# Kernel optimization log

Measured on AMD Instinct MI355X. Metric: run time of the kernel, lower is better.

Reference implementation:

```python
import jax, jax.numpy as jnp
import numpy as np

N = 4
IS_SLOW = (False, False, True, True)
RATES = (1, 1, 4, 4)
THRESH = 0.3
F2S_IDX = {(0, 2): 0, (0, 3): 1, (1, 2): 2, (1, 3): 3}


def _conv1d(x, w, stride, pad):
    # x: [B, C_in, T], w: [C_out, C_in, K]
    return jax.lax.conv_general_dilated(
        x, w, (stride,), [(pad, pad)], dimension_numbers=("NCH", "OIH", "NCH"))


def _linear_interp(x, t_out):
    # x: [B, D, T_in] -> [B, D, t_out]; matches F.interpolate(mode='linear', align_corners=False)
    t_in = x.shape[2]
    scale = t_in / t_out
    src = (jnp.arange(t_out, dtype=jnp.float32) + 0.5) * scale - 0.5
    src = jnp.clip(src, 0.0, float(t_in - 1))
    i0 = jnp.floor(src).astype(jnp.int32)
    i1 = jnp.minimum(i0 + 1, t_in - 1)
    w = (src - i0.astype(jnp.float32)).astype(x.dtype)
    return x[:, :, i0] * (1.0 - w) + x[:, :, i1] * w


def setup_inputs() -> dict:
    key = jax.random.key(0)
    ks = jax.random.split(key, 8)
    T_FAST, T_SLOW, B, D, H = 512, 128, 32, 1024, 256
    return {
        "feat0": jax.random.normal(ks[0], (T_FAST, B, D), jnp.float32),
        "feat1": jax.random.normal(ks[1], (T_FAST, B, D), jnp.float32),
        "feat2": jax.random.normal(ks[2], (T_SLOW, B, D), jnp.float32),
        "feat3": jax.random.normal(ks[3], (T_SLOW, B, D), jnp.float32),
        "mlp_w1": jax.random.normal(ks[4], (N * N, 2 * D, H), jnp.float32) * 0.02,
        "mlp_b1": jnp.zeros((N * N, H), jnp.float32),
        "mlp_w2": jax.random.normal(ks[5], (N * N, H, 1), jnp.float32) * 0.02,
        "mlp_b2": jnp.zeros((N * N, 1), jnp.float32),
        "s2f_w": jax.random.normal(ks[6], (D, D, 1), jnp.float32) * 0.02,
        "s2f_b": jnp.zeros((D,), jnp.float32),
        "f2s_w": jax.random.normal(ks[7], (4, D, D, 5), jnp.float32) * 0.02,
    }


def reference(feat0, feat1, feat2, feat3, mlp_w1, mlp_b1, mlp_w2, mlp_b2,
              s2f_w, s2f_b, f2s_w):
    feats = [feat0, feat1, feat2, feat3]            # [T_i, B, D]
    feats_bdt = [jnp.transpose(f, (1, 2, 0)) for f in feats]  # [B, D, T_i]
    globals_ = [f.mean(axis=2) for f in feats_bdt]  # [B, D]
    outputs = list(feats)
    for i in range(N):
        for j in range(N):
            if i == j:
                continue
            p = i * N + j
            pair_vec = jnp.concatenate([globals_[i], globals_[j]], axis=-1)  # [B, 2D]
            h = jax.nn.relu(pair_vec @ mlp_w1[p] + mlp_b1[p])
            score = jax.nn.sigmoid(h @ mlp_w2[p] + mlp_b2[p])[:, 0]          # [B]
            cond = score.mean() >= THRESH
            if IS_SLOW[i] and not IS_SLOW[j]:
                # slow -> fast: interpolate up, 1x1 conv proj, score-weighted residual
                up = _linear_interp(feats_bdt[i], feats_bdt[j].shape[2])
                up = _conv1d(up, s2f_w, 1, 0) + s2f_b[None, :, None]
                new = feats_bdt[j] + score[:, None, None] * up
                outputs[j] = jnp.where(cond, jnp.transpose(new, (2, 0, 1)), outputs[j])
            elif (not IS_SLOW[i]) and IS_SLOW[j]:
                # fast -> slow: strided conv down, score-weighted residual
                stride = RATES[j] // RATES[i]
                down = _conv1d(feats_bdt[i], f2s_w[F2S_IDX[(i, j)]], stride, 2)
                new = feats_bdt[j] + score[:, None, None] * down
                outputs[j] = jnp.where(cond, jnp.transpose(new, (2, 0, 1)), outputs[j])
    return tuple(outputs)
```

## Files before the change

### kernel.cpp

```cpp
#include <hip/hip_runtime.h>
#include <math.h>

typedef __bf16 bf16;
typedef bf16 bf16x8 __attribute__((ext_vector_type(8)));
typedef bf16 bf16x4 __attribute__((ext_vector_type(4)));
typedef float f32x4 __attribute__((ext_vector_type(4)));

#define OFF_GLOB   0ul
#define OFF_H      524288ul
#define OFF_SCORE  786432ul
#define OFF_COND   787456ul
#define OFF_PART   788480ul
#define OFF_PROJ   4982784ul
#define OFF_WTF2S  38537216ul
#define OFF_WTS2F  59508736ul
#define OFF_F0B    61605888ul
#define OFF_F1B    95160320ul
#define OFF_F2B    128714752ul
#define OFF_F3B    137103360ul
#define WS_NEED    145491968ul


__device__ __forceinline__ void slot_ij(int s, int& i, int& j) {
  if (s < 4) { i = 2 + (s & 1); j = s >> 1; }
  else       { int ss = s - 4; i = ss & 1; j = 2 + (ss >> 1); }
}

__global__ __launch_bounds__(256) void k_means_part(
    const float* __restrict__ f0, const float* __restrict__ f1,
    const float* __restrict__ f2, const float* __restrict__ f3,
    float* __restrict__ part,
    bf16* __restrict__ b0, bf16* __restrict__ b1,
    bf16* __restrict__ b2, bf16* __restrict__ b3, int do_conv)
{
  int b = blockIdx.x, c = blockIdx.y, i = blockIdx.z, tid = threadIdx.x;
  const float* f = (i == 0) ? f0 : (i == 1) ? f1 : (i == 2) ? f2 : f3;
  bf16* fb = (i == 0) ? b0 : (i == 1) ? b1 : (i == 2) ? b2 : b3;
  int chunk = (i < 2) ? 64 : 16;
  int t0 = c * chunk;
  float4 s = make_float4(0.f, 0.f, 0.f, 0.f);
  for (int t = t0; t < t0 + chunk; ++t) {
    float4 v = ((const float4*)(f + (size_t)(t * 32 + b) * 1024))[tid];
    s.x += v.x; s.y += v.y; s.z += v.z; s.w += v.w;
    if (do_conv) {
      bf16x4 o;
      o[0] = (bf16)v.x; o[1] = (bf16)v.y; o[2] = (bf16)v.z; o[3] = (bf16)v.w;
      *(bf16x4*)(fb + (size_t)(t * 32 + b) * 1024 + tid * 4) = o;
    }
  }
  ((float4*)part)[(size_t)((i * 8 + c) * 32 + b) * 256 + tid] = s;
}

__global__ __launch_bounds__(256) void k_means_final(
    const float* __restrict__ part, float* __restrict__ g)
{
  int b = blockIdx.x, i = blockIdx.y, tid = threadIdx.x;
  float4 s = make_float4(0.f, 0.f, 0.f, 0.f);
  for (int c = 0; c < 8; ++c) {
    float4 v = ((const float4*)part)[(size_t)((i * 8 + c) * 32 + b) * 256 + tid];
    s.x += v.x; s.y += v.y; s.z += v.z; s.w += v.w;
  }
  float inv = (i < 2) ? (1.f / 512.f) : (1.f / 128.f);
  s.x *= inv; s.y *= inv; s.z *= inv; s.w *= inv;
  ((float4*)g)[(size_t)(i * 32 + b) * 256 + tid] = s;
}

__global__ __launch_bounds__(256) void k_mlp1(
    const float* __restrict__ g, const float* __restrict__ w1, float* __restrict__ h_ws)
{
  int s = blockIdx.x, hc = blockIdx.y, kz = blockIdx.z, tid = threadIdx.x;
  int pi, pj; slot_ij(s, pi, pj);
  int p = pi * 4 + pj;
  int h = hc * 32 + (tid & 31);
  int bg = tid >> 5;
  __shared__ float pv[32 * 65];
  float acc0 = 0.f, acc1 = 0.f, acc2 = 0.f, acc3 = 0.f;
  for (int kt = 0; kt < 8; ++kt) {
    int k0 = kz * 512 + kt * 64;
    __syncthreads();
    for (int l = tid; l < 2048; l += 256) {
      int bb = l >> 6, kk = l & 63;
      int k = k0 + kk;
      float v = (k < 1024) ? g[(size_t)pi * 32768 + bb * 1024 + k]
                           : g[(size_t)pj * 32768 + bb * 1024 + (k - 1024)];
      pv[bb * 65 + kk] = v;
    }
    __syncthreads();
    const float* wp = w1 + ((size_t)p * 2048 + k0) * 256 + hc * 32 + (tid & 31);
    for (int kk = 0; kk < 64; ++kk) {
      float w = wp[(size_t)kk * 256];
      acc0 += pv[(bg * 4 + 0) * 65 + kk] * w;
      acc1 += pv[(bg * 4 + 1) * 65 + kk] * w;
      acc2 += pv[(bg * 4 + 2) * 65 + kk] * w;
      acc3 += pv[(bg * 4 + 3) * 65 + kk] * w;
    }
  }
  atomicAdd(&h_ws[(size_t)s * 8192 + (bg * 4 + 0) * 256 + h], acc0);
  atomicAdd(&h_ws[(size_t)s * 8192 + (bg * 4 + 1) * 256 + h], acc1);
  atomicAdd(&h_ws[(size_t)s * 8192 + (bg * 4 + 2) * 256 + h], acc2);
  atomicAdd(&h_ws[(size_t)s * 8192 + (bg * 4 + 3) * 256 + h], acc3);
}

__global__ __launch_bounds__(256) void k_mlp2(
    const float* __restrict__ h_ws, const float* __restrict__ b1,
    const float* __restrict__ w2, const float* __restrict__ b2,
    float* __restrict__ score, float* __restrict__ cond)
{
  int s = blockIdx.x, tid = threadIdx.x;
  int pi, pj; slot_ij(s, pi, pj);
  int p = pi * 4 + pj;
  float w2v = w2[p * 256 + tid];
  float b1v = b1[p * 256 + tid];
  float b2v = b2[p];
  __shared__ float red[4];
  float tot = 0.f;
  for (int b = 0; b < 32; ++b) {
    float v = fmaxf(h_ws[(size_t)s * 8192 + b * 256 + tid] + b1v, 0.f) * w2v;
    for (int off = 32; off > 0; off >>= 1) v += __shfl_down(v, off);
    if ((tid & 63) == 0) red[tid >> 6] = v;
    __syncthreads();
    if (tid == 0) {
      float sum = red[0] + red[1] + red[2] + red[3] + b2v;
      float sc = 1.f / (1.f + expf(-sum));
      score[s * 32 + b] = sc;
      tot += sc;
    }
    __syncthreads();
  }
  if (tid == 0) cond[s] = (tot * (1.f / 32.f) >= 0.3f) ? 1.f : 0.f;
}

__global__ __launch_bounds__(256) void k_f2s_transpose(
    const float* __restrict__ w, const float* __restrict__ cond, bf16* __restrict__ wT)
{
  int z = blockIdx.y, co = blockIdx.x, tid = threadIdx.x;
  int sel = (cond[5 + 2 * z] > 0.5f) ? 1 : ((cond[4 + 2 * z] > 0.5f) ? 0 : -1);
  if (sel < 0) return;
  int widx = sel * 2 + z;
  __shared__ float buf[5120];
  const float* src = w + ((size_t)widx * 1024 + co) * 5120;
  for (int l = tid; l < 5120; l += 256) buf[l] = src[l];
  __syncthreads();
  bf16* dst = wT + (size_t)z * 5242880 + (size_t)co * 5120;
  for (int o = tid; o < 5120; o += 256) {
    int kk = o >> 10, ci = o & 1023;
    dst[o] = (bf16)buf[ci * 5 + kk];
  }
}

__global__ __launch_bounds__(256) void k_s2f_convert(
    const float* __restrict__ w, bf16* __restrict__ wT)
{
  size_t gi = (size_t)blockIdx.x * 256 + threadIdx.x;
  float4 v = ((const float4*)w)[gi];
  bf16x4 o;
  o[0] = (bf16)v.x; o[1] = (bf16)v.y; o[2] = (bf16)v.z; o[3] = (bf16)v.w;
  *(bf16x4*)&wT[gi * 4] = o;
}

template<bool PRE>
__global__ __launch_bounds__(256) void k_s2f_gemm(
    const float* __restrict__ feat2, const float* __restrict__ feat3,
    const bf16* __restrict__ f2b, const bf16* __restrict__ f3b,
    const bf16* __restrict__ wT, const float* __restrict__ s2f_b,
    const float* __restrict__ cond, float* __restrict__ proj)
{
  int z = blockIdx.z;
  int sel = (cond[1 + 2 * z] > 0.5f) ? 3 : ((cond[2 * z] > 0.5f) ? 2 : -1);
  if (sel < 0) return;
  const float* A = (sel == 3) ? feat3 : feat2;
  const bf16* Ab = (sel == 3) ? f3b : f2b;
  float* projz = proj + (size_t)z * 4194304;
  int tid = threadIdx.x;
  int lin = blockIdx.y * 32 + blockIdx.x;
  int o_ = (lin & 7) * 32 + (lin >> 3);
  int M0 = (o_ & 31) * 128, N0 = (o_ >> 5) * 128;
  __shared__ bf16 As[128][72];
  __shared__ bf16 Bs[128][72];
  f32x4 acc[4][4];
  for (int a = 0; a < 4; ++a)
    for (int c = 0; c < 4; ++c) { acc[a][c][0] = 0.f; acc[a][c][1] = 0.f; acc[a][c][2] = 0.f; acc[a][c][3] = 0.f; }
  int row = tid >> 1, half = tid & 1;
  int lane = tid & 63, wv = tid >> 6;
  int wr = (wv >> 1) * 64, wc = (wv & 1) * 64;
  int rl = lane & 15, q = lane >> 4;
  for (int kt = 0; kt < 16; ++kt) {
    int ci0 = kt * 64;
    __syncthreads();
    if (PRE) {
      const uint4* src = (const uint4*)(Ab + (size_t)(M0 + row) * 1024 + ci0 + half * 32);
      #pragma unroll
      for (int u = 0; u < 4; ++u) *(uint4*)&As[row][half * 32 + u * 8] = src[u];
    } else {
      const float4* src = (const float4*)(A + (size_t)(M0 + row) * 1024 + ci0 + half * 32);
      #pragma unroll
      for (int u = 0; u < 4; ++u) {
        float4 v0 = src[2 * u], v1 = src[2 * u + 1];
        bf16x8 pk;
        pk[0] = (bf16)v0.x; pk[1] = (bf16)v0.y; pk[2] = (bf16)v0.z; pk[3] = (bf16)v0.w;
        pk[4] = (bf16)v1.x; pk[5] = (bf16)v1.y; pk[6] = (bf16)v1.z; pk[7] = (bf16)v1.w;
        *(bf16x8*)&As[row][half * 32 + u * 8] = pk;
      }
    }
    {
      const uint4* bs = (const uint4*)(wT + (size_t)(N0 + row) * 1024 + ci0 + half * 32);
      #pragma unroll
      for (int u = 0; u < 4; ++u) *(uint4*)&Bs[row][half * 32 + u * 8] = bs[u];
    }
    __syncthreads();
    #pragma unroll
    for (int ks = 0; ks < 2; ++ks) {
      bf16x8 af[4], bfv[4];
      #pragma unroll
      for (int mi = 0; mi < 4; ++mi) af[mi] = *(const bf16x8*)&As[wr + mi * 16 + rl][ks * 32 + q * 8];
      #pragma unroll
      for (int ni = 0; ni < 4; ++ni) bfv[ni] = *(const bf16x8*)&Bs[wc + ni * 16 + rl][ks * 32 + q * 8];
      #pragma unroll
      for (int mi = 0; mi < 4; ++mi)
        #pragma unroll
        for (int ni = 0; ni < 4; ++ni)
          acc[mi][ni] = __builtin_amdgcn_mfma_f32_16x16x32_bf16(af[mi], bfv[ni], acc[mi][ni], 0, 0, 0);
    }
  }
  #pragma unroll
  for (int mi = 0; mi < 4; ++mi)
    #pragma unroll
    for (int ni = 0; ni < 4; ++ni)
      #pragma unroll
      for (int r = 0; r < 4; ++r) {
        int gm = M0 + wr + mi * 16 + q * 4 + r;
        int gn = N0 + wc + ni * 16 + rl;
        projz[(size_t)gm * 1024 + gn] = acc[mi][ni][r] + s2f_b[gn];
      }
}

template<bool PRE>
__global__ __launch_bounds__(256) void k_f2s_gemm(
    const float* __restrict__ feat0, const float* __restrict__ feat1,
    const bf16* __restrict__ f0b, const bf16* __restrict__ f1b,
    const float* __restrict__ feat2, const float* __restrict__ feat3,
    const bf16* __restrict__ wT, const float* __restrict__ score,
    const float* __restrict__ cond, float* __restrict__ out)
{
  int z = blockIdx.z;
  const float* fj = z ? feat3 : feat2;
  float* oj = out + 33554432ul + (size_t)z * 4194304;
  int tid = threadIdx.x;
  int lin = blockIdx.y * 32 + blockIdx.x;
  int o_ = (lin & 7) * 32 + (lin >> 3);
  int M0 = (o_ & 31) * 128, N0 = (o_ >> 5) * 128;
  int sel = (cond[5 + 2 * z] > 0.5f) ? 1 : ((cond[4 + 2 * z] > 0.5f) ? 0 : -1);
  if (sel < 0) {
    for (int l = tid; l < 4096; l += 256) {
      int rr = l >> 5, c4 = l & 31;
      size_t idx = (size_t)(M0 + rr) * 1024 + N0 + c4 * 4;
      *(float4*)(oj + idx) = *(const float4*)(fj + idx);
    }
    return;
  }
  const float* A = sel ? feat1 : feat0;
  const bf16* Ab = sel ? f1b : f0b;
  const bf16* wTz = wT + (size_t)z * 5242880;
  int slot = (sel ? 5 : 4) + 2 * z;
  __shared__ bf16 As[128][72];
  __shared__ bf16 Bs[128][72];
  __shared__ float sld[32];
  if (tid < 32) sld[tid] = score[slot * 32 + tid];
  f32x4 acc[4][4];
  for (int a = 0; a < 4; ++a)
    for (int c = 0; c < 4; ++c) { acc[a][c][0] = 0.f; acc[a][c][1] = 0.f; acc[a][c][2] = 0.f; acc[a][c][3] = 0.f; }
  int row = tid >> 1, half = tid & 1;
  int m = M0 + row, t = m >> 5, b = m & 31;
  int lane = tid & 63, wv = tid >> 6;
  int wr = (wv >> 1) * 64, wc = (wv & 1) * 64;
  int rl = lane & 15, q = lane >> 4;
  for (int kt = 0; kt < 80; ++kt) {
    int kk = kt >> 4, ci0 = (kt & 15) << 6;
    int pos = 4 * t - 2 + kk;
    __syncthreads();
    if (PRE) {
      uint4 v[4];
      if (pos >= 0) {
        const uint4* src = (const uint4*)(Ab + (size_t)(pos * 32 + b) * 1024 + ci0 + half * 32);
        #pragma unroll
        for (int u = 0; u < 4; ++u) v[u] = src[u];
      } else {
        #pragma unroll
        for (int u = 0; u < 4; ++u) v[u] = make_uint4(0u, 0u, 0u, 0u);
      }
      #pragma unroll
      for (int u = 0; u < 4; ++u) *(uint4*)&As[row][half * 32 + u * 8] = v[u];
    } else {
      float4 v[8];
      if (pos >= 0 && pos < 512) {
        const float4* src = (const float4*)(A + (size_t)(pos * 32 + b) * 1024 + ci0 + half * 32);
        #pragma unroll
        for (int u = 0; u < 8; ++u) v[u] = src[u];
      } else {
        #pragma unroll
        for (int u = 0; u < 8; ++u) v[u] = make_float4(0.f, 0.f, 0.f, 0.f);
      }
      #pragma unroll
      for (int u = 0; u < 4; ++u) {
        bf16x8 pk;
        pk[0] = (bf16)v[2 * u].x; pk[1] = (bf16)v[2 * u].y; pk[2] = (bf16)v[2 * u].z; pk[3] = (bf16)v[2 * u].w;
        pk[4] = (bf16)v[2 * u + 1].x; pk[5] = (bf16)v[2 * u + 1].y; pk[6] = (bf16)v[2 * u + 1].z; pk[7] = (bf16)v[2 * u + 1].w;
        *(bf16x8*)&As[row][half * 32 + u * 8] = pk;
      }
    }
    {
      const uint4* bs = (const uint4*)(wTz + (size_t)(N0 + row) * 5120 + kt * 64 + half * 32);
      #pragma unroll
      for (int u = 0; u < 4; ++u) *(uint4*)&Bs[row][half * 32 + u * 8] = bs[u];
    }
    __syncthreads();
    #pragma unroll
    for (int ks = 0; ks < 2; ++ks) {
      bf16x8 af[4], bfv[4];
      #pragma unroll
      for (int mi = 0; mi < 4; ++mi) af[mi] = *(const bf16x8*)&As[wr + mi * 16 + rl][ks * 32 + q * 8];
      #pragma unroll
      for (int ni = 0; ni < 4; ++ni) bfv[ni] = *(const bf16x8*)&Bs[wc + ni * 16 + rl][ks * 32 + q * 8];
      #pragma unroll
      for (int mi = 0; mi < 4; ++mi)
        #pragma unroll
        for (int ni = 0; ni < 4; ++ni)
          acc[mi][ni] = __builtin_amdgcn_mfma_f32_16x16x32_bf16(af[mi], bfv[ni], acc[mi][ni], 0, 0, 0);
    }
  }
  #pragma unroll
  for (int mi = 0; mi < 4; ++mi)
    #pragma unroll
    for (int ni = 0; ni < 4; ++ni)
      #pragma unroll
      for (int r = 0; r < 4; ++r) {
        int gm = M0 + wr + mi * 16 + q * 4 + r;
        int gn = N0 + wc + ni * 16 + rl;
        size_t idx = (size_t)gm * 1024 + gn;
        oj[idx] = fj[idx] + sld[gm & 31] * acc[mi][ni][r];
      }
}

__global__ __launch_bounds__(256) void k_interp(
    const float* __restrict__ f0, const float* __restrict__ f1,
    const float* __restrict__ proj, const float* __restrict__ score,
    const float* __restrict__ cond, float* __restrict__ out)
{
  int z = blockIdx.y, tb = blockIdx.x, tid = threadIdx.x;
  const float* fj = z ? f1 : f0;
  float* oj = out + (size_t)z * 16777216;
  int sel = (cond[1 + 2 * z] > 0.5f) ? 3 : ((cond[2 * z] > 0.5f) ? 2 : -1);
  float4 fv = ((const float4*)(fj + (size_t)tb * 1024))[tid];
  if (sel < 0) {
    ((float4*)(oj + (size_t)tb * 1024))[tid] = fv;
    return;
  }
  int t = tb >> 5, b = tb & 31;
  int slot = 2 * z + (sel == 3 ? 1 : 0);
  float s = score[slot * 32 + b];
  float srcf = 0.25f * (float)t - 0.375f;
  srcf = fminf(fmaxf(srcf, 0.f), 127.f);
  int i0 = (int)srcf;
  int i1 = min(i0 + 1, 127);
  float w = srcf - (float)i0;
  const float* pz = proj + (size_t)z * 4194304;
  float4 a = ((const float4*)(pz + (size_t)(i0 * 32 + b) * 1024))[tid];
  float4 c = ((const float4*)(pz + (size_t)(i1 * 32 + b) * 1024))[tid];
  float4 o;
  o.x = fv.x + s * ((1.f - w) * a.x + w * c.x);
  o.y = fv.y + s * ((1.f - w) * a.y + w * c.y);
  o.z = fv.z + s * ((1.f - w) * a.z + w * c.z);
  o.w = fv.w + s * ((1.f - w) * a.w + w * c.w);
  ((float4*)(oj + (size_t)tb * 1024))[tid] = o;
}

extern "C" void kernel_launch(void* const* d_in, const int* in_sizes, int n_in,
                              void* d_out, int out_size, void* d_ws, size_t ws_size,
                              hipStream_t stream) {
  const float* f0   = (const float*)d_in[0];
  const float* f1   = (const float*)d_in[1];
  const float* f2   = (const float*)d_in[2];
  const float* f3   = (const float*)d_in[3];
  const float* w1   = (const float*)d_in[4];
  const float* b1   = (const float*)d_in[5];
  const float* w2   = (const float*)d_in[6];
  const float* b2   = (const float*)d_in[7];
  const float* s2fw = (const float*)d_in[8];
  const float* s2fb = (const float*)d_in[9];
  const float* f2sw = (const float*)d_in[10];
  float* out = (float*)d_out;

  char* ws = (char*)d_ws;
  float* g     = (float*)(ws + OFF_GLOB);
  float* h_ws  = (float*)(ws + OFF_H);
  float* score = (float*)(ws + OFF_SCORE);
  float* cond  = (float*)(ws + OFF_COND);
  float* part  = (float*)(ws + OFF_PART);
  float* proj  = (float*)(ws + OFF_PROJ);
  bf16*  wtf   = (bf16*)(ws + OFF_WTF2S);
  bf16*  wts   = (bf16*)(ws + OFF_WTS2F);
  bf16*  f0b   = (bf16*)(ws + OFF_F0B);
  bf16*  f1b   = (bf16*)(ws + OFF_F1B);
  bf16*  f2b   = (bf16*)(ws + OFF_F2B);
  bf16*  f3b   = (bf16*)(ws + OFF_F3B);

  const bool pre = (ws_size >= WS_NEED);

  hipMemsetAsync(h_ws, 0, 262144, stream);
  if (pre)
    k_means_part<<<dim3(32, 8, 4), 256, 0, stream>>>(f0, f1, f2, f3, part, f0b, f1b, f2b, f3b, 1);
  else
    k_means_part<<<dim3(32, 8, 4), 256, 0, stream>>>(f0, f1, f2, f3, part,
                                                     (bf16*)nullptr, (bf16*)nullptr,
                                                     (bf16*)nullptr, (bf16*)nullptr, 0);
  k_means_final<<<dim3(32, 4), 256, 0, stream>>>(part, g);
  k_mlp1<<<dim3(8, 8, 4), 256, 0, stream>>>(g, w1, h_ws);
  k_mlp2<<<8, 256, 0, stream>>>(h_ws, b1, w2, b2, score, cond);
  k_f2s_transpose<<<dim3(1024, 2), 256, 0, stream>>>(f2sw, cond, wtf);
  k_s2f_convert<<<1024, 256, 0, stream>>>(s2fw, wts);
  if (pre) {
    k_s2f_gemm<true><<<dim3(32, 8, 2), 256, 0, stream>>>(f2, f3, f2b, f3b, wts, s2fb, cond, proj);
    k_f2s_gemm<true><<<dim3(32, 8, 2), 256, 0, stream>>>(f0, f1, f0b, f1b, f2, f3, wtf, score, cond, out);
  } else {
    k_s2f_gemm<false><<<dim3(32, 8, 2), 256, 0, stream>>>(f2, f3, f2b, f3b, wts, s2fb, cond, proj);
    k_f2s_gemm<false><<<dim3(32, 8, 2), 256, 0, stream>>>(f0, f1, f0b, f1b, f2, f3, wtf, score, cond, out);
  }
  k_interp<<<dim3(16384, 2), 256, 0, stream>>>(f0, f1, proj, score, cond, out);
}
```

Measured before the change: 641.4 us.

## Double-buffer GEMM tiles with direct global-to-LDS loads and XOR swizzle

The bf16 pre-converted GEMM paths for both the slow-to-fast projection and the fast-to-slow strided conv are rewritten to use global_load_lds with a two-stage LDS ping-pong, so the next K tile is fetched while MFMAs run on the current one. The shared tiles drop padding in favor of an XOR swizzle to avoid bank conflicts, and out-of-range conv taps read from a small zeroed buffer instead of branching. The MLP score kernel is also changed to let each wave handle eight batches with float4 loads, removing per-batch block barriers. This costs twice the LDS per block, which may reduce occupancy.

```diff
diff --git a/kernel.cpp b/kernel.cpp
--- a/kernel.cpp
+++ b/kernel.cpp
@@ -1,5 +1,6 @@
 #include <hip/hip_runtime.h>
 #include <math.h>
+#include <stdint.h>
 
 typedef __bf16 bf16;
 typedef bf16 bf16x8 __attribute__((ext_vector_type(8)));
@@ -20,6 +21,11 @@
 #define OFF_F3B    137103360ul
 #define WS_NEED    145491968ul
 
+__device__ __forceinline__ void gl2lds16(const void* g, void* lds) {
+  __builtin_amdgcn_global_load_lds(
+      (const __attribute__((address_space(1))) unsigned int*)g,
+      (__attribute__((address_space(3))) unsigned int*)lds, 16, 0, 0);
+}
 
 __device__ __forceinline__ void slot_ij(int s, int& i, int& j) {
   if (s < 4) { i = 2 + (s & 1); j = s >> 1; }
@@ -109,25 +115,31 @@
   int s = blockIdx.x, tid = threadIdx.x;
   int pi, pj; slot_ij(s, pi, pj);
   int p = pi * 4 + pj;
-  float w2v = w2[p * 256 + tid];
-  float b1v = b1[p * 256 + tid];
+  int lane = tid & 63, wv = tid >> 6;
+  float4 w2v = ((const float4*)(w2 + p * 256))[lane];
+  float4 b1v = ((const float4*)(b1 + p * 256))[lane];
   float b2v = b2[p];
-  __shared__ float red[4];
+  __shared__ float redw[4];
   float tot = 0.f;
-  for (int b = 0; b < 32; ++b) {
-    float v = fmaxf(h_ws[(size_t)s * 8192 + b * 256 + tid] + b1v, 0.f) * w2v;
+  for (int bb = 0; bb < 8; ++bb) {
+    int b = wv * 8 + bb;
+    float4 h4 = ((const float4*)(h_ws + (size_t)s * 8192 + b * 256))[lane];
+    float v = fmaxf(h4.x + b1v.x, 0.f) * w2v.x + fmaxf(h4.y + b1v.y, 0.f) * w2v.y
+            + fmaxf(h4.z + b1v.z, 0.f) * w2v.z + fmaxf(h4.w + b1v.w, 0.f) * w2v.w;
+    #pragma unroll
     for (int off = 32; off > 0; off >>= 1) v += __shfl_down(v, off);
-    if ((tid & 63) == 0) red[tid >> 6] = v;
-    __syncthreads();
-    if (tid == 0) {
-      float sum = red[0] + red[1] + red[2] + red[3] + b2v;
-      float sc = 1.f / (1.f + expf(-sum));
+    if (lane == 0) {
+      float sc = 1.f / (1.f + expf(-(v + b2v)));
       score[s * 32 + b] = sc;
       tot += sc;
     }
-    __syncthreads();
-  }
-  if (tid == 0) cond[s] = (tot * (1.f / 32.f) >= 0.3f) ? 1.f : 0.f;
+  }
+  if (lane == 0) redw[wv] = tot;
+  __syncthreads();
+  if (tid == 0) {
+    float t = redw[0] + redw[1] + redw[2] + redw[3];
+    cond[s] = (t * (1.f / 32.f) >= 0.3f) ? 1.f : 0.f;
+  }
 }
 
 __global__ __launch_bounds__(256) void k_f2s_transpose(
@@ -158,10 +170,194 @@
   *(bf16x4*)&wT[gi * 4] = o;
 }
 
-template<bool PRE>
-__global__ __launch_bounds__(256) void k_s2f_gemm(
+
+__global__ __launch_bounds__(256) void k_s2f_gemm2(
+    const bf16* __restrict__ f2b, const bf16* __restrict__ f3b,
+    const bf16* __restrict__ wT, const float* __restrict__ s2f_b,
+    const float* __restrict__ cond, float* __restrict__ proj)
+{
+  int z = blockIdx.z;
+  int sel = (cond[1 + 2 * z] > 0.5f) ? 3 : ((cond[2 * z] > 0.5f) ? 2 : -1);
+  if (sel < 0) return;
+  const bf16* Ab = (sel == 3) ? f3b : f2b;
+  float* projz = proj + (size_t)z * 4194304;
+  int tid = threadIdx.x;
+  int lin = blockIdx.y * 32 + blockIdx.x;
+  int o_ = (lin & 7) * 32 + (lin >> 3);
+  int M0 = (o_ & 31) * 128, N0 = (o_ >> 5) * 128;
+  __shared__ bf16 As[2][8192];
+  __shared__ bf16 Bs[2][8192];
+  f32x4 acc[4][4];
+  #pragma unroll
+  for (int a = 0; a < 4; ++a)
+    #pragma unroll
+    for (int c = 0; c < 4; ++c) { acc[a][c][0] = 0.f; acc[a][c][1] = 0.f; acc[a][c][2] = 0.f; acc[a][c][3] = 0.f; }
+  int lane = tid & 63, wv = tid >> 6;
+  int wr = (wv >> 1) * 64, wc = (wv & 1) * 64;
+  int rl = lane & 15, q = lane >> 4;
+  int wb = tid & 192;
+
+  size_t aoffs[4], boffs[4];
+  #pragma unroll
+  for (int rnd = 0; rnd < 4; ++rnd) {
+    int c = rnd * 256 + tid, lr = c >> 3, seg = c & 7, sw = seg ^ (lr & 7);
+    aoffs[rnd] = (size_t)(M0 + lr) * 1024 + sw * 8;
+    boffs[rnd] = (size_t)(N0 + lr) * 1024 + sw * 8;
+  }
+
+  #define S2F_STAGE(KT, PB) {                                        \
+    size_t ci0 = (size_t)(KT) * 64;                                  \
+    _Pragma("unroll")                                                \
+    for (int rnd = 0; rnd < 4; ++rnd) {                              \
+      gl2lds16(Ab + aoffs[rnd] + ci0, &As[PB][(rnd * 256 + wb) * 8]);\
+      gl2lds16(wT + boffs[rnd] + ci0, &Bs[PB][(rnd * 256 + wb) * 8]);\
+    } }
+
+  S2F_STAGE(0, 0);
+  __syncthreads();
+  for (int kt = 0; kt < 16; ++kt) {
+    int pb = kt & 1;
+    if (kt < 15) S2F_STAGE(kt + 1, pb ^ 1);
+    const bf16* Ac = &As[pb][0];
+    const bf16* Bc = &Bs[pb][0];
+    #pragma unroll
+    for (int ks = 0; ks < 2; ++ks) {
+      bf16x8 af[4], bfv[4];
+      #pragma unroll
+      for (int mi = 0; mi < 4; ++mi) {
+        int r = wr + mi * 16 + rl;
+        af[mi] = *(const bf16x8*)&Ac[r * 64 + (((ks << 2) + q) ^ (r & 7)) * 8];
+      }
+      #pragma unroll
+      for (int ni = 0; ni < 4; ++ni) {
+        int r = wc + ni * 16 + rl;
+        bfv[ni] = *(const bf16x8*)&Bc[r * 64 + (((ks << 2) + q) ^ (r & 7)) * 8];
+      }
+      #pragma unroll
+      for (int mi = 0; mi < 4; ++mi)
+        #pragma unroll
+        for (int ni = 0; ni < 4; ++ni)
+          acc[mi][ni] = __builtin_amdgcn_mfma_f32_16x16x32_bf16(af[mi], bfv[ni], acc[mi][ni], 0, 0, 0);
+    }
+    __syncthreads();
+  }
+  #pragma unroll
+  for (int mi = 0; mi < 4; ++mi)
+    #pragma unroll
+    for (int ni = 0; ni < 4; ++ni)
+      #pragma unroll
+      for (int r = 0; r < 4; ++r) {
+        int gm = M0 + wr + mi * 16 + q * 4 + r;
+        int gn = N0 + wc + ni * 16 + rl;
+        projz[(size_t)gm * 1024 + gn] = acc[mi][ni][r] + s2f_b[gn];
+      }
+}
+
+__global__ __launch_bounds__(256) void k_f2s_gemm2(
+    const bf16* __restrict__ f0b, const bf16* __restrict__ f1b,
     const float* __restrict__ feat2, const float* __restrict__ feat3,
-    const bf16* __restrict__ f2b, const bf16* __restrict__ f3b,
+    const bf16* __restrict__ wT, const float* __restrict__ score,
+    const float* __restrict__ cond, const bf16* __restrict__ zbuf,
+    float* __restrict__ out)
+{
+  int z = blockIdx.z;
+  const float* fj = z ? feat3 : feat2;
+  float* oj = out + 33554432ul + (size_t)z * 4194304;
+  int tid = threadIdx.x;
+  int lin = blockIdx.y * 32 + blockIdx.x;
+  int o_ = (lin & 7) * 32 + (lin >> 3);
+  int M0 = (o_ & 31) * 128, N0 = (o_ >> 5) * 128;
+  int sel = (cond[5 + 2 * z] > 0.5f) ? 1 : ((cond[4 + 2 * z] > 0.5f) ? 0 : -1);
+  if (sel < 0) {
+    for (int l = tid; l < 4096; l += 256) {
+      int rr = l >> 5, c4 = l & 31;
+      size_t idx = (size_t)(M0 + rr) * 1024 + N0 + c4 * 4;
+      *(float4*)(oj + idx) = *(const float4*)(fj + idx);
+    }
+    return;
+  }
+  const bf16* Ab = sel ? f1b : f0b;
+  const bf16* wTz = wT + (size_t)z * 5242880;
+  int slot = (sel ? 5 : 4) + 2 * z;
+  __shared__ bf16 As[2][8192];
+  __shared__ bf16 Bs[2][8192];
+  __shared__ float sld[32];
+  if (tid < 32) sld[tid] = score[slot * 32 + tid];
+  f32x4 acc[4][4];
+  #pragma unroll
+  for (int a = 0; a < 4; ++a)
+    #pragma unroll
+    for (int c = 0; c < 4; ++c) { acc[a][c][0] = 0.f; acc[a][c][1] = 0.f; acc[a][c][2] = 0.f; acc[a][c][3] = 0.f; }
+  int lane = tid & 63, wv = tid >> 6;
+  int wr = (wv >> 1) * 64, wc = (wv & 1) * 64;
+  int rl = lane & 15, q = lane >> 4;
+  int wb = tid & 192;
+
+  long aoffs[4]; size_t boffs[4]; bool t0f[4];
+  #pragma unroll
+  for (int rnd = 0; rnd < 4; ++rnd) {
+    int c = rnd * 256 + tid, lr = c >> 3, seg = c & 7, sw = seg ^ (lr & 7);
+    int m = M0 + lr, t = m >> 5, b = m & 31;
+    aoffs[rnd] = ((long)(4 * t - 2) * 32 + b) * 1024 + sw * 8;
+    t0f[rnd] = (t == 0);
+    boffs[rnd] = (size_t)(N0 + lr) * 5120 + sw * 8;
+  }
+
+  #define F2S_STAGE(KT, PB) {                                                   \
+    int kk_ = (KT) >> 4;                                                        \
+    long aadd_ = (long)kk_ * 32768 + (((KT) & 15) << 6);                        \
+    size_t badd_ = (size_t)(KT) * 64;                                           \
+    bool zk_ = (kk_ < 2);                                                       \
+    _Pragma("unroll")                                                           \
+    for (int rnd = 0; rnd < 4; ++rnd) {                                         \
+      const bf16* sA = (zk_ && t0f[rnd]) ? zbuf : (Ab + aoffs[rnd] + aadd_);    \
+      gl2lds16(sA, &As[PB][(rnd * 256 + wb) * 8]);                              \
+      gl2lds16(wTz + boffs[rnd] + badd_, &Bs[PB][(rnd * 256 + wb) * 8]);        \
+    } }
+
+  F2S_STAGE(0, 0);
+  __syncthreads();
+  for (int kt = 0; kt < 80; ++kt) {
+    int pb = kt & 1;
+    if (kt < 79) F2S_STAGE(kt + 1, pb ^ 1);
+    const bf16* Ac = &As[pb][0];
+    const bf16* Bc = &Bs[pb][0];
+    #pragma unroll
+    for (int ks = 0; ks < 2; ++ks) {
+      bf16x8 af[4], bfv[4];
+      #pragma unroll
+      for (int mi = 0; mi < 4; ++mi) {
+        int r = wr + mi * 16 + rl;
+        af[mi] = *(const bf16x8*)&Ac[r * 64 + (((ks << 2) + q) ^ (r & 7)) * 8];
+      }
+      #pragma unroll
+      for (int ni = 0; ni < 4; ++ni) {
+        int r = wc + ni * 16 + rl;
+        bfv[ni] = *(const bf16x8*)&Bc[r * 64 + (((ks << 2) + q) ^ (r & 7)) * 8];
+      }
+      #pragma unroll
+      for (int mi = 0; mi < 4; ++mi)
+        #pragma unroll
+        for (int ni = 0; ni < 4; ++ni)
+          acc[mi][ni] = __builtin_amdgcn_mfma_f32_16x16x32_bf16(af[mi], bfv[ni], acc[mi][ni], 0, 0, 0);
+    }
+    __syncthreads();
+  }
+  #pragma unroll
+  for (int mi = 0; mi < 4; ++mi)
+    #pragma unroll
+    for (int ni = 0; ni < 4; ++ni)
+      #pragma unroll
+      for (int r = 0; r < 4; ++r) {
+        int gm = M0 + wr + mi * 16 + q * 4 + r;
+        int gn = N0 + wc + ni * 16 + rl;
+        size_t idx = (size_t)gm * 1024 + gn;
+        oj[idx] = fj[idx] + sld[gm & 31] * acc[mi][ni][r];
+      }
+}
+
+__global__ __launch_bounds__(256) void k_s2f_gemm_fb(
+    const float* __restrict__ feat2, const float* __restrict__ feat3,
     const bf16* __restrict__ wT, const float* __restrict__ s2f_b,
     const float* __restrict__ cond, float* __restrict__ proj)
 {
@@ -169,7 +365,6 @@
   int sel = (cond[1 + 2 * z] > 0.5f) ? 3 : ((cond[2 * z] > 0.5f) ? 2 : -1);
   if (sel < 0) return;
   const float* A = (sel == 3) ? feat3 : feat2;
-  const bf16* Ab = (sel == 3) ? f3b : f2b;
   float* projz = proj + (size_t)z * 4194304;
   int tid = threadIdx.x;
   int lin = blockIdx.y * 32 + blockIdx.x;
@@ -187,11 +382,7 @@
   for (int kt = 0; kt < 16; ++kt) {
     int ci0 = kt * 64;
     __syncthreads();
-    if (PRE) {
-      const uint4* src = (const uint4*)(Ab + (size_t)(M0 + row) * 1024 + ci0 + half * 32);
-      #pragma unroll
-      for (int u = 0; u < 4; ++u) *(uint4*)&As[row][half * 32 + u * 8] = src[u];
-    } else {
+    {
       const float4* src = (const float4*)(A + (size_t)(M0 + row) * 1024 + ci0 + half * 32);
       #pragma unroll
       for (int u = 0; u < 4; ++u) {
@@ -201,8 +392,6 @@
         pk[4] = (bf16)v1.x; pk[5] = (bf16)v1.y; pk[6] = (bf16)v1.z; pk[7] = (bf16)v1.w;
         *(bf16x8*)&As[row][half * 32 + u * 8] = pk;
       }
-    }
-    {
       const uint4* bs = (const uint4*)(wT + (size_t)(N0 + row) * 1024 + ci0 + half * 32);
       #pragma unroll
       for (int u = 0; u < 4; ++u) *(uint4*)&Bs[row][half * 32 + u * 8] = bs[u];
@@ -234,10 +423,8 @@
       }
 }
 
-template<bool PRE>
-__global__ __launch_bounds__(256) void k_f2s_gemm(
+__global__ __launch_bounds__(256) void k_f2s_gemm_fb(
     const float* __restrict__ feat0, const float* __restrict__ feat1,
-    const bf16* __restrict__ f0b, const bf16* __restrict__ f1b,
     const float* __restrict__ feat2, const float* __restrict__ feat3,
     const bf16* __restrict__ wT, const float* __restrict__ score,
     const float* __restrict__ cond, float* __restrict__ out)
@@ -259,7 +446,6 @@
     return;
   }
   const float* A = sel ? feat1 : feat0;
-  const bf16* Ab = sel ? f1b : f0b;
   const bf16* wTz = wT + (size_t)z * 5242880;
   int slot = (sel ? 5 : 4) + 2 * z;
   __shared__ bf16 As[128][72];
@@ -278,19 +464,7 @@
     int kk = kt >> 4, ci0 = (kt & 15) << 6;
     int pos = 4 * t - 2 + kk;
     __syncthreads();
-    if (PRE) {
-      uint4 v[4];
-      if (pos >= 0) {
-        const uint4* src = (const uint4*)(Ab + (size_t)(pos * 32 + b) * 1024 + ci0 + half * 32);
-        #pragma unroll
-        for (int u = 0; u < 4; ++u) v[u] = src[u];
-      } else {
-        #pragma unroll
-        for (int u = 0; u < 4; ++u) v[u] = make_uint4(0u, 0u, 0u, 0u);
-      }
-      #pragma unroll
-      for (int u = 0; u < 4; ++u) *(uint4*)&As[row][half * 32 + u * 8] = v[u];
-    } else {
+    {
       float4 v[8];
       if (pos >= 0 && pos < 512) {
         const float4* src = (const float4*)(A + (size_t)(pos * 32 + b) * 1024 + ci0 + half * 32);
@@ -307,8 +481,6 @@
         pk[4] = (bf16)v[2 * u + 1].x; pk[5] = (bf16)v[2 * u + 1].y; pk[6] = (bf16)v[2 * u + 1].z; pk[7] = (bf16)v[2 * u + 1].w;
         *(bf16x8*)&As[row][half * 32 + u * 8] = pk;
       }
-    }
-    {
       const uint4* bs = (const uint4*)(wTz + (size_t)(N0 + row) * 5120 + kt * 64 + half * 32);
       #pragma unroll
       for (int u = 0; u < 4; ++u) *(uint4*)&Bs[row][half * 32 + u * 8] = bs[u];
@@ -395,6 +567,7 @@
   float* h_ws  = (float*)(ws + OFF_H);
   float* score = (float*)(ws + OFF_SCORE);
   float* cond  = (float*)(ws + OFF_COND);
+  bf16*  zbuf  = (bf16*)(ws + OFF_COND + 256);
   float* part  = (float*)(ws + OFF_PART);
   float* proj  = (float*)(ws + OFF_PROJ);
   bf16*  wtf   = (bf16*)(ws + OFF_WTF2S);
@@ -407,6 +580,7 @@
   const bool pre = (ws_size >= WS_NEED);
 
   hipMemsetAsync(h_ws, 0, 262144, stream);
+  hipMemsetAsync(ws + OFF_COND + 256, 0, 64, stream);
   if (pre)
     k_means_part<<<dim3(32, 8, 4), 256, 0, stream>>>(f0, f1, f2, f3, part, f0b, f1b, f2b, f3b, 1);
   else
@@ -419,11 +593,11 @@
   k_f2s_transpose<<<dim3(1024, 2), 256, 0, stream>>>(f2sw, cond, wtf);
   k_s2f_convert<<<1024, 256, 0, stream>>>(s2fw, wts);
   if (pre) {
-    k_s2f_gemm<true><<<dim3(32, 8, 2), 256, 0, stream>>>(f2, f3, f2b, f3b, wts, s2fb, cond, proj);
-    k_f2s_gemm<true><<<dim3(32, 8, 2), 256, 0, stream>>>(f0, f1, f0b, f1b, f2, f3, wtf, score, cond, out);
+    k_s2f_gemm2<<<dim3(32, 8, 2), 256, 0, stream>>>(f2b, f3b, wts, s2fb, cond, proj);
+    k_f2s_gemm2<<<dim3(32, 8, 2), 256, 0, stream>>>(f0b, f1b, f2, f3, wtf, score, cond, zbuf, out);
   } else {
-    k_s2f_gemm<false><<<dim3(32, 8, 2), 256, 0, stream>>>(f2, f3, f2b, f3b, wts, s2fb, cond, proj);
-    k_f2s_gemm<false><<<dim3(32, 8, 2), 256, 0, stream>>>(f0, f1, f0b, f1b, f2, f3, wtf, score, cond, out);
+    k_s2f_gemm_fb<<<dim3(32, 8, 2), 256, 0, stream>>>(f2, f3, wts, s2fb, cond, proj);
+    k_f2s_gemm_fb<<<dim3(32, 8, 2), 256, 0, stream>>>(f0, f1, f2, f3, wtf, score, cond, out);
   }
   k_interp<<<dim3(16384, 2), 256, 0, stream>>>(f0, f1, proj, score, cond, out);
 }
```

After: 626.3 us. 2.4% less time.
